# Kernel optimization log

Measured on AMD Instinct MI355X. Metric: run time of the kernel, lower is better.

The kernel has to match this reference:

```python
import jax, jax.numpy as jnp
import numpy as np

NCOLS = 32768   # number of independent water columns (batched)
NZ = 64         # vertical levels per column
NT = 40         # time steps
DT = 30.0       # time step [s]
GAMMA_COR = 0.55


def _edge(val, like):
    return jnp.reshape(jnp.asarray(val, like.dtype), (1,))


def add_boundaries(btm, interior, sfc):
    return jnp.concatenate([_edge(btm, interior), interior, _edge(sfc, interior)])


def tridiag_solve(a, b, c, f):
    # Thomas algorithm: forward elimination then back substitution.
    def fwd(carry, abcf):
        cp_prev, dp_prev = carry
        ai, bi, ci, fi = abcf
        denom = bi - ai * cp_prev
        cp = ci / denom
        dp = (fi - ai * dp_prev) / denom
        return (cp, dp), (cp, dp)

    zero = jnp.zeros((), a.dtype)
    _, (cp, dp) = jax.lax.scan(fwd, (zero, zero), (a, b, c, f))

    def bwd(x_next, cd):
        cpi, dpi = cd
        x = dpi - cpi * x_next
        return x, x

    _, x = jax.lax.scan(bwd, zero, (cp, dp), reverse=True)
    return x


def diffusion_solver(ak, hz, f, dt):
    a_in = -2.0 * dt * ak[1:-2] / (hz[:-2] + hz[1:-1])
    c_in = -2.0 * dt * ak[2:-1] / (hz[2:] + hz[1:-1])
    b_in = hz[1:-1] - a_in - c_in
    c_btm = -2.0 * dt * ak[1] / (hz[1] + hz[0])
    b_btm = hz[0] - c_btm
    a_sfc = -2.0 * dt * ak[-2] / (hz[-2] + hz[-1])
    b_sfc = hz[-1] - a_sfc
    a = add_boundaries(0.0, a_in, a_sfc)
    b = add_boundaries(b_btm, b_in, b_sfc)
    c = add_boundaries(c_btm, c_in, 0.0)
    return tridiag_solve(a, b, c, f)


_solve = jax.vmap(lambda ak, hz, f: diffusion_solver(ak, hz, f, DT))


def setup_inputs() -> dict:
    key = jax.random.key(0)
    ks = jax.random.split(key, 14)
    sh = (NCOLS, NZ)
    u0 = 0.1 * jax.random.normal(ks[0], sh, jnp.float32)
    v0 = 0.1 * jax.random.normal(ks[1], sh, jnp.float32)
    t0 = 15.0 + jax.random.normal(ks[2], sh, jnp.float32)
    s0 = 35.0 + 0.1 * jax.random.normal(ks[3], sh, jnp.float32)
    hz = jax.random.uniform(ks[4], sh, jnp.float32, 0.5, 2.0)
    akv = jax.random.uniform(ks[5], (NCOLS, NZ + 1), jnp.float32, 1e-4, 1e-2)
    akt = jax.random.uniform(ks[6], (NCOLS, NZ + 1), jnp.float32, 1e-4, 1e-2)
    t_forcing = 1e-5 * jax.random.normal(ks[7], sh, jnp.float32)
    s_forcing = 1e-6 * jax.random.normal(ks[8], sh, jnp.float32)
    ustr_sfc = 1e-4 * jax.random.normal(ks[9], (NCOLS,), jnp.float32)
    vstr_sfc = 1e-4 * jax.random.normal(ks[10], (NCOLS,), jnp.float32)
    ustr_btm = 1e-5 * jax.random.normal(ks[11], (NCOLS,), jnp.float32)
    vstr_btm = 1e-5 * jax.random.normal(ks[12], (NCOLS,), jnp.float32)
    fcor = jax.random.uniform(ks[13], (NCOLS,), jnp.float32, 5e-5, 1.5e-4)
    return {"u0": u0, "v0": v0, "t0": t0, "s0": s0, "hz": hz, "akv": akv,
            "akt": akt, "t_forcing": t_forcing, "s_forcing": s_forcing,
            "ustr_sfc": ustr_sfc, "vstr_sfc": vstr_sfc,
            "ustr_btm": ustr_btm, "vstr_btm": vstr_btm, "fcor": fcor}


def reference(u0, v0, t0, s0, hz, akv, akt, t_forcing, s_forcing,
              ustr_sfc, vstr_sfc, ustr_btm, vstr_btm, fcor):
    dtf = jnp.float32(DT)
    cff = (dtf * fcor) ** 2                                   # [ncols]
    cff1 = 1.0 / (1.0 + GAMMA_COR * GAMMA_COR * cff)
    coef = 1.0 - GAMMA_COR * (1.0 - GAMMA_COR) * cff
    dtfc = (dtf * fcor)[:, None]
    cff1b, coefb = cff1[:, None], coef[:, None]

    @jax.checkpoint
    def step(carry, _):
        u, v, t, s = carry
        # advance_tra_ed: tracer diffusion with constant-type forcing
        t = _solve(akt, hz, hz * t + dtf * t_forcing)
        s = _solve(akt, hz, hz * s + dtf * s_forcing)
        # advance_dyn_cor_ed: semi-implicit Coriolis + stress BCs + diffusion
        fu = cff1b * hz * (coefb * u + dtfc * v)
        fv = cff1b * hz * (coefb * v - dtfc * u)
        fu = fu.at[:, -1].add(dtf * ustr_sfc).at[:, 0].add(-dtf * ustr_btm)
        fv = fv.at[:, -1].add(dtf * vstr_sfc).at[:, 0].add(-dtf * vstr_btm)
        u = _solve(akv, hz, fu)
        v = _solve(akv, hz, fv)
        return (u, v, t, s), None

    (u, v, t, s), _ = jax.lax.scan(step, (u0, v0, t0, s0), None, length=NT)
    return jnp.stack([u, v, t, s])  # [4, ncols, nz]
```

## Files before the change

kernel.cpp:

```cpp
#include <hip/hip_runtime.h>
#include <hip/hip_bf16.h>

#define NCOLS 32768
#define NZ 64
#define NT 40
#define DTF 30.0f
#define GAMMAC 0.55f

typedef _Float16 f16;

#define SBAR() __builtin_amdgcn_sched_barrier(0)

__device__ __forceinline__ float dpp_swap1(float x) {
    return __int_as_float(__builtin_amdgcn_mov_dpp(__float_as_int(x), 0xB1, 0xF, 0xF, true));
}
__device__ __forceinline__ unsigned int packh2(float a, float b) {
    union { f16 h[2]; unsigned int u; } v;
    v.h[0] = (f16)a; v.h[1] = (f16)b; return v.u;
}
__device__ __forceinline__ unsigned short f16bits(float a) {
    union { f16 h; unsigned short u; } v; v.h = (f16)a; return v.u;
}
__device__ __forceinline__ float lo16f(unsigned int x) {
    union { unsigned int u; f16 h[2]; } v; v.u = x; return (float)v.h[0];
}
__device__ __forceinline__ float hi16f(unsigned int x) {
    union { unsigned int u; f16 h[2]; } v; v.u = x; return (float)v.h[1];
}

__global__ __launch_bounds__(256, 2) void scm_kernel(
    const float* __restrict__ u0, const float* __restrict__ v0,
    const float* __restrict__ t0, const float* __restrict__ s0,
    const float* __restrict__ hz, const float* __restrict__ akv,
    const float* __restrict__ akt, const float* __restrict__ tfo,
    const float* __restrict__ sfo, const float* __restrict__ uss,
    const float* __restrict__ vss, const float* __restrict__ usb,
    const float* __restrict__ vsb, const float* __restrict__ fcor,
    float* __restrict__ out)
{
    __shared__ uint4 Wsh[16 * 128];
    __shared__ uint4 CP4sh[8 * 128];
    __shared__ uint4 FG4sh[8 * 256];

    const int ltid  = threadIdx.x;
    const int tid   = blockIdx.x * 256 + ltid;
    const int field = tid & 3;
    const int col   = tid >> 2;
    const int p     = ltid >> 1;

    const float* ak  = (field < 2) ? akv : akt;
    const float* st0 = (field == 0) ? u0 : (field == 1) ? v0 : (field == 2) ? t0 : s0;

    float walpha = 1.0f, rcor = 0.0f;
    {
        float fc   = fcor[col];
        float dtfc = DTF * fc;
        float cff  = dtfc * dtfc;
        float cff1 = 1.0f / (1.0f + GAMMAC * GAMMAC * cff);
        float coefc = 1.0f - GAMMAC * (1.0f - GAMMAC) * cff;
        if (field == 0)      { walpha = cff1 * coefc; rcor =  dtfc / coefc; }
        else if (field == 1) { walpha = cff1 * coefc; rcor = -dtfc / coefc; }
    }

    float bnd0 = 0.f, bnd63 = 0.f;
    if (field == 0)      { bnd0 = -DTF * usb[col]; bnd63 = DTF * uss[col]; }
    else if (field == 1) { bnd0 = -DTF * vsb[col]; bnd63 = DTF * vss[col]; }

    const float* hzc = hz + (size_t)col * NZ;
    const float* akc = ak + (size_t)col * (NZ + 1);
    const float* fr  = (field >= 2) ? (((field == 2) ? tfo : sfo) + (size_t)col * NZ)
                                    : hzc;

    {
        float cpprev = 0.f, aik = 0.f, hk = hzc[0];
        uint4 wacc = {}; uint4 c8 = {}, f8 = {};
        #pragma unroll
        for (int k = 0; k < NZ; ++k) {
            float hk1 = 0.f, aik1 = 0.f;
            float frv = fr[k];
            if (k < NZ - 1) {
                hk1  = hzc[k + 1];
                aik1 = (-2.0f * DTF) * akc[k + 1] / (hk + hk1);
            }
            float bk    = hk - aik - aik1;
            float denom = bk - aik * cpprev;
            float g     = 1.0f / denom;
            float cpk   = aik1 * g;
            float fgk;
            if (field >= 2) fgk = (DTF * frv) * g;
            else            fgk = (k == 0 ? bnd0 : (k == NZ - 1 ? bnd63 : 0.0f)) * g;
            unsigned int   wv = packh2(hk * g * walpha, -aik * g);
            unsigned short cv = f16bits(-cpk);
            unsigned short fv = f16bits(fgk);
            switch (k & 7) {
                case 0: wacc.x = wv; c8.x = cv; f8.x = fv; break;
                case 1: wacc.y = wv; c8.x |= ((unsigned)cv << 16);
                        f8.x |= ((unsigned)fv << 16); break;
                case 2: wacc.z = wv; c8.y = cv; f8.y = fv; break;
                case 3: wacc.w = wv; c8.y |= ((unsigned)cv << 16);
                        f8.y |= ((unsigned)fv << 16);
                        if ((ltid & 1) == 0) Wsh[(k >> 2) * 128 + p] = wacc;
                        break;
                case 4: wacc.x = wv; c8.z = cv; f8.z = fv; break;
                case 5: wacc.y = wv; c8.z |= ((unsigned)cv << 16);
                        f8.z |= ((unsigned)fv << 16); break;
                case 6: wacc.z = wv; c8.w = cv; f8.w = fv; break;
                default:
                    wacc.w = wv; c8.w |= ((unsigned)cv << 16);
                    f8.w |= ((unsigned)fv << 16);
                    FG4sh[(k >> 3) * 256 + ltid] = f8;
                    if ((ltid & 1) == 0) {
                        Wsh[(k >> 2) * 128 + p]   = wacc;
                        CP4sh[(k >> 3) * 128 + p] = c8;
                    }
                    break;
            }
            cpprev = cpk; aik = aik1; hk = hk1;
            if ((k & 15) == 15) SBAR();
        }
    }

    float tau[NZ];
    {
        const float4* sp = (const float4*)(st0 + (size_t)col * NZ);
        #pragma unroll
        for (int k4 = 0; k4 < NZ / 4; ++k4) {
            float4 s = sp[k4];
            tau[4*k4+0] = s.x; tau[4*k4+1] = s.y;
            tau[4*k4+2] = s.z; tau[4*k4+3] = s.w;
        }
    }

    float meanadd = 0.0f;
    if (field >= 2) {
        float ssum = 0.f;
        #pragma unroll
        for (int k = 0; k < NZ; ++k) ssum += tau[k];
        meanadd = ssum * (1.0f / NZ);
        #pragma unroll
        for (int k = 0; k < NZ; ++k) tau[k] -= meanadd;
    }

    __syncthreads();

    for (int n = 0; n < NT; ++n) {
        float dpprev = 0.f;
        uint4 f8;
        #pragma unroll
        for (int q = 0; q < 16; ++q) {
            uint4 w = Wsh[q * 128 + p];
            if ((q & 1) == 0) f8 = FG4sh[(q >> 1) * 256 + ltid];
            #pragma unroll
            for (int i = 0; i < 4; ++i) {
                unsigned wv = (i == 0) ? w.x : (i == 1) ? w.y
                            : (i == 2) ? w.z : w.w;
                const int sel = ((q & 1) << 1) | (i >> 1);
                unsigned fgw = (sel == 0) ? f8.x : (sel == 1) ? f8.y
                             : (sel == 2) ? f8.z : f8.w;
                float fgv = (i & 1) ? hi16f(fgw) : lo16f(fgw);
                float own = tau[4*q + i];
                float oth = dpp_swap1(own);
                float m   = fmaf(rcor, oth, own);
                float dp  = fmaf(lo16f(wv), m, fgv);
                dp = fmaf(hi16f(wv), dpprev, dp);
                tau[4*q + i] = dp;
                dpprev = dp;
            }
            if ((q & 3) == 3) SBAR();
        }
        float xn = 0.f;
        uint4 c8;
        #pragma unroll
        for (int q = 15; q >= 0; --q) {
            if ((q & 1) == 1) c8 = CP4sh[(q >> 1) * 128 + p];
            #pragma unroll
            for (int i = 3; i >= 0; --i) {
                const int sel = ((q & 1) << 1) | (i >> 1);
                unsigned cw = (sel == 0) ? c8.x : (sel == 1) ? c8.y
                            : (sel == 2) ? c8.z : c8.w;
                float cv = (i & 1) ? hi16f(cw) : lo16f(cw);
                float x = fmaf(cv, xn, tau[4*q + i]);
                tau[4*q + i] = x;
                xn = x;
            }
            if ((q & 3) == 0) SBAR();
        }
    }

    float* op = out + ((size_t)field * NCOLS + col) * NZ;
    #pragma unroll
    for (int k4 = 0; k4 < NZ / 4; ++k4) {
        float4 w;
        w.x = tau[4*k4+0] + meanadd;
        w.y = tau[4*k4+1] + meanadd;
        w.z = tau[4*k4+2] + meanadd;
        w.w = tau[4*k4+3] + meanadd;
        ((float4*)op)[k4] = w;
    }
}

extern "C" void kernel_launch(void* const* d_in, const int* in_sizes, int n_in,
                              void* d_out, int out_size, void* d_ws, size_t ws_size,
                              hipStream_t stream) {
    const float* u0   = (const float*)d_in[0];
    const float* v0   = (const float*)d_in[1];
    const float* t0   = (const float*)d_in[2];
    const float* s0   = (const float*)d_in[3];
    const float* hz   = (const float*)d_in[4];
    const float* akv  = (const float*)d_in[5];
    const float* akt  = (const float*)d_in[6];
    const float* tfo  = (const float*)d_in[7];
    const float* sfo  = (const float*)d_in[8];
    const float* uss  = (const float*)d_in[9];
    const float* vss  = (const float*)d_in[10];
    const float* usb  = (const float*)d_in[11];
    const float* vsb  = (const float*)d_in[12];
    const float* fcor = (const float*)d_in[13];

    scm_kernel<<<dim3((NCOLS * 4) / 256), dim3(256), 0, stream>>>(
        u0, v0, t0, s0, hz, akv, akt, tfo, sfo, uss, vss, usb, vsb, fcor,
        (float*)d_out);
}
```

Before: 87.39 us.

## Eliminate tracer forcing term via particular-solution decomposition of constant forcing

For the tracer fields, the constant forcing is split analytically into a per-step uniform mean increase (mu) plus a stationary particular profile. The profile is computed once from prefix sums and subtracted from the state before time stepping, then added back at the end. This removes the FG4sh shared-memory buffer and its per-step loads from the forward sweep. Only the boundary-stress addends remain, at levels 0 and 63, as scalars. The profile is stashed temporarily in the output buffer, and the decomposition may change float rounding compared with direct forcing.

```diff
diff --git a/kernel.cpp b/kernel.cpp
--- a/kernel.cpp
+++ b/kernel.cpp
@@ -40,15 +40,15 @@
 {
     __shared__ uint4 Wsh[16 * 128];
     __shared__ uint4 CP4sh[8 * 128];
-    __shared__ uint4 FG4sh[8 * 256];
 
     const int ltid  = threadIdx.x;
     const int tid   = blockIdx.x * 256 + ltid;
     const int field = tid & 3;
     const int col   = tid >> 2;
     const int p     = ltid >> 1;
-
-    const float* ak  = (field < 2) ? akv : akt;
+    const bool isTS = (field >= 2);
+
+    const float* ak  = isTS ? akt : akv;
     const float* st0 = (field == 0) ? u0 : (field == 1) ? v0 : (field == 2) ? t0 : s0;
 
     float walpha = 1.0f, rcor = 0.0f;
@@ -68,12 +68,14 @@
 
     const float* hzc = hz + (size_t)col * NZ;
     const float* akc = ak + (size_t)col * (NZ + 1);
-    const float* fr  = (field >= 2) ? (((field == 2) ? tfo : sfo) + (size_t)col * NZ)
-                                    : hzc;
-
+    const float* fr  = isTS ? (((field == 2) ? tfo : sfo) + (size_t)col * NZ)
+                            : hzc;
+    float* op = out + ((size_t)field * NCOLS + col) * NZ;
+
+    float gb0 = 0.f, gb63 = 0.f, Sf = 0.f, Sh = 0.f;
     {
         float cpprev = 0.f, aik = 0.f, hk = hzc[0];
-        uint4 wacc = {}; uint4 c8 = {}, f8 = {};
+        uint4 wacc = {}; uint4 c8 = {};
         #pragma unroll
         for (int k = 0; k < NZ; ++k) {
             float hk1 = 0.f, aik1 = 0.f;
@@ -82,33 +84,28 @@
                 hk1  = hzc[k + 1];
                 aik1 = (-2.0f * DTF) * akc[k + 1] / (hk + hk1);
             }
+            Sf += DTF * frv;
+            Sh += hk;
             float bk    = hk - aik - aik1;
             float denom = bk - aik * cpprev;
             float g     = 1.0f / denom;
             float cpk   = aik1 * g;
-            float fgk;
-            if (field >= 2) fgk = (DTF * frv) * g;
-            else            fgk = (k == 0 ? bnd0 : (k == NZ - 1 ? bnd63 : 0.0f)) * g;
+            if (k == 0)      gb0  = bnd0  * g;
+            if (k == NZ - 1) gb63 = bnd63 * g;
             unsigned int   wv = packh2(hk * g * walpha, -aik * g);
             unsigned short cv = f16bits(-cpk);
-            unsigned short fv = f16bits(fgk);
             switch (k & 7) {
-                case 0: wacc.x = wv; c8.x = cv; f8.x = fv; break;
-                case 1: wacc.y = wv; c8.x |= ((unsigned)cv << 16);
-                        f8.x |= ((unsigned)fv << 16); break;
-                case 2: wacc.z = wv; c8.y = cv; f8.y = fv; break;
+                case 0: wacc.x = wv; c8.x = cv; break;
+                case 1: wacc.y = wv; c8.x |= ((unsigned)cv << 16); break;
+                case 2: wacc.z = wv; c8.y = cv; break;
                 case 3: wacc.w = wv; c8.y |= ((unsigned)cv << 16);
-                        f8.y |= ((unsigned)fv << 16);
                         if ((ltid & 1) == 0) Wsh[(k >> 2) * 128 + p] = wacc;
                         break;
-                case 4: wacc.x = wv; c8.z = cv; f8.z = fv; break;
-                case 5: wacc.y = wv; c8.z |= ((unsigned)cv << 16);
-                        f8.z |= ((unsigned)fv << 16); break;
-                case 6: wacc.z = wv; c8.w = cv; f8.w = fv; break;
+                case 4: wacc.x = wv; c8.z = cv; break;
+                case 5: wacc.y = wv; c8.z |= ((unsigned)cv << 16); break;
+                case 6: wacc.z = wv; c8.w = cv; break;
                 default:
                     wacc.w = wv; c8.w |= ((unsigned)cv << 16);
-                    f8.w |= ((unsigned)fv << 16);
-                    FG4sh[(k >> 3) * 256 + ltid] = f8;
                     if ((ltid & 1) == 0) {
                         Wsh[(k >> 2) * 128 + p]   = wacc;
                         CP4sh[(k >> 3) * 128 + p] = c8;
@@ -119,6 +116,7 @@
             if ((k & 15) == 15) SBAR();
         }
     }
+    const float mu = isTS ? (Sf / Sh) : 0.0f;
 
     float tau[NZ];
     {
@@ -131,8 +129,32 @@
         }
     }
 
+    {
+        float pv = 0.f, Pf = 0.f, Ph = 0.f;
+        float4 pac;
+        #pragma unroll
+        for (int k = 0; k < NZ; ++k) {
+            if ((k & 3) == 0) pac.x = pv;
+            else if ((k & 3) == 1) pac.y = pv;
+            else if ((k & 3) == 2) pac.z = pv;
+            else {
+                pac.w = pv;
+                if (isTS) ((float4*)op)[k >> 2] = pac;
+            }
+            if (isTS) tau[k] -= pv;
+            float hk = hzc[k];
+            Pf += DTF * fr[k];
+            Ph += hk;
+            if (k < NZ - 1) {
+                float num = fmaf(-mu, Ph, Pf) * (hk + hzc[k + 1]);
+                pv += num / ((-2.0f * DTF) * akc[k + 1]);
+            }
+            if ((k & 15) == 15) SBAR();
+        }
+    }
+
     float meanadd = 0.0f;
-    if (field >= 2) {
+    if (isTS) {
         float ssum = 0.f;
         #pragma unroll
         for (int k = 0; k < NZ; ++k) ssum += tau[k];
@@ -145,25 +167,21 @@
 
     for (int n = 0; n < NT; ++n) {
         float dpprev = 0.f;
-        uint4 f8;
         #pragma unroll
         for (int q = 0; q < 16; ++q) {
             uint4 w = Wsh[q * 128 + p];
-            if ((q & 1) == 0) f8 = FG4sh[(q >> 1) * 256 + ltid];
             #pragma unroll
             for (int i = 0; i < 4; ++i) {
+                const int k = 4*q + i;
                 unsigned wv = (i == 0) ? w.x : (i == 1) ? w.y
                             : (i == 2) ? w.z : w.w;
-                const int sel = ((q & 1) << 1) | (i >> 1);
-                unsigned fgw = (sel == 0) ? f8.x : (sel == 1) ? f8.y
-                             : (sel == 2) ? f8.z : f8.w;
-                float fgv = (i & 1) ? hi16f(fgw) : lo16f(fgw);
-                float own = tau[4*q + i];
+                float addend = (k == 0) ? gb0 : (k == NZ - 1) ? gb63 : 0.0f;
+                float own = tau[k];
                 float oth = dpp_swap1(own);
                 float m   = fmaf(rcor, oth, own);
-                float dp  = fmaf(lo16f(wv), m, fgv);
-                dp = fmaf(hi16f(wv), dpprev, dp);
-                tau[4*q + i] = dp;
+                float t   = fmaf(lo16f(wv), m, addend);
+                float dp  = fmaf(hi16f(wv), dpprev, t);
+                tau[k] = dp;
                 dpprev = dp;
             }
             if ((q & 3) == 3) SBAR();
@@ -187,14 +205,16 @@
         }
     }
 
-    float* op = out + ((size_t)field * NCOLS + col) * NZ;
+    const float base = meanadd + (float)NT * mu;
     #pragma unroll
     for (int k4 = 0; k4 < NZ / 4; ++k4) {
+        float4 pv = make_float4(0.f, 0.f, 0.f, 0.f);
+        if (isTS) pv = ((float4*)op)[k4];
         float4 w;
-        w.x = tau[4*k4+0] + meanadd;
-        w.y = tau[4*k4+1] + meanadd;
-        w.z = tau[4*k4+2] + meanadd;
-        w.w = tau[4*k4+3] + meanadd;
+        w.x = tau[4*k4+0] + base + pv.x;
+        w.y = tau[4*k4+1] + base + pv.y;
+        w.z = tau[4*k4+2] + base + pv.z;
+        w.w = tau[4*k4+3] + base + pv.w;
         ((float4*)op)[k4] = w;
     }
 }
```

Result: slower. 111.8 us (+27.9%).
